# Kernel optimization log

Measured on AMD Instinct MI355X. Metric: run time of the kernel, lower is better.

The kernel has to match this reference:

```python
import jax, jax.numpy as jnp
from jax import lax
import numpy as np

P1, P2, M1, M2, WIN, STEP = 7, 7, 18, 55, 37, 4


def _unfold(x, p):
    # x: [N,C,Hp,Wp] -> [N, C*p*p, Ho*Wo], torch.nn.functional.unfold ordering (C, di, dj)
    N, C, Hp, Wp = x.shape
    Ho, Wo = Hp - p + 1, Wp - p + 1
    cols = jnp.stack([x[:, :, i:i + Ho, j:j + Wo] for i in range(p) for j in range(p)], axis=2)
    return cols.reshape(N, C * p * p, Ho * Wo)


def _reflect_unfold(x, r, p):
    return _unfold(jnp.pad(x, ((0, 0), (0, 0), (r, r), (r, r)), mode='reflect'), p)


def _fold(X, p, oh, ow):
    # inverse of unfold (sum of overlapping patches), torch.nn.functional.fold
    N, n, L = X.shape
    Ho, Wo = oh - p + 1, ow - p + 1
    C = n // (p * p)
    Xr = X.reshape(N, C, p, p, Ho, Wo)
    out = jnp.zeros((N, C, oh, ow), X.dtype)
    for i in range(p):
        for j in range(p):
            out = out.at[:, :, i:i + Ho, j:j + Wo].add(Xr[:, :, i, j])
    return out


def _block_matching(x, m, p, w, s):
    # x: [N,1,H,W] -> flat patch indices [N, B*m] into the (H+w-1)x(W+w-1) unfold grid
    N, C, H, Wd = x.shape
    inc = w // 2
    xs = _reflect_unfold(x, p // 2 + inc, p).reshape(N, p * p, H + 2 * inc, Wd + 2 * inc)
    xc = xs[:, :, inc:inc + H:s, inc:inc + Wd:s]  # [N, p*p, Hs, Ws]
    Hs, Ws = xc.shape[2], xc.shape[3]
    offs = jnp.stack(jnp.meshgrid(jnp.arange(w), jnp.arange(w), indexing='ij'), axis=-1).reshape(-1, 2)
    def d_of(off):
        xo = lax.dynamic_slice(xs, (0, 0, off[0], off[1]), (N, p * p, H, Wd))[:, :, ::s, ::s]
        return jnp.sum((xo - xc) ** 2, axis=1)  # [N, Hs, Ws]
    dist = jnp.moveaxis(lax.map(d_of, offs), 0, 1)  # [N, w*w, Hs, Ws]
    dist = dist.at[:, inc * w + inc].set(-1.0)  # force self-match first
    _, idx = lax.top_k(-jnp.transpose(dist, (0, 2, 3, 1)), m)  # smallest m, sorted
    idx = jnp.transpose(idx, (0, 3, 1, 2))  # [N, m, Hs, Ws]
    ir = idx // w - inc
    ic = idx % w - inc
    rows = inc + s * jnp.arange(Hs)
    cols = inc + s * jnp.arange(Ws)
    flat = (ir + rows[None, None, :, None]) * (Wd + w - 1) + (ic + cols[None, None, None, :])
    return jnp.transpose(flat.reshape(N, m, Hs * Ws), (0, 2, 1)).reshape(N, -1)  # [N, B*m]


def _group_patches(unf, idx, m, n):
    # unf: [N, n, L], idx: [N, B*m] -> [N, B, m, n]
    N = unf.shape[0]
    g = jnp.take_along_axis(unf, idx[:, None, :], axis=2)  # [N, n, B*m]
    return jnp.transpose(g, (0, 2, 1)).reshape(N, -1, m, n)


def _denoise1(Y, sigma):
    m, n = Y.shape[2], Y.shape[3]
    YtY = jnp.einsum('abik,abjk->abij', Y, Y)
    rhs = YtY - (n * sigma ** 2) * jnp.eye(m, dtype=Y.dtype)
    theta = jnp.swapaxes(jnp.linalg.solve(YtY, rhs), -1, -2)
    Xh = theta @ Y
    wts = 1.0 / jnp.sum(theta ** 2, axis=3, keepdims=True)
    return Xh, wts


def _denoise2(Y, X, sigma):
    m, n = X.shape[2], X.shape[3]
    XtX = jnp.einsum('abik,abjk->abij', X, X)
    A = XtX + (n * sigma ** 2) * jnp.eye(m, dtype=X.dtype)
    theta = jnp.swapaxes(jnp.linalg.solve(A, XtX), -1, -2)
    Xh = theta @ Y
    wts = 1.0 / jnp.sum(theta ** 2, axis=3, keepdims=True)
    return Xh, wts


def _aggregation(Y, wts, idx, H, Wd, L, p, w):
    # Y: [N,B,m,n], wts: [N,B,m,1], idx: [N,B*m]; scatter-add into unfold grid, fold, normalize
    N, B, m, n = Y.shape
    Yw = jnp.transpose(Y * wts, (0, 3, 1, 2)).reshape(N, n, B * m)
    wflat = jnp.broadcast_to(wts.reshape(N, 1, B * m), (N, n, B * m))
    def scat(vals, ib):
        return jnp.zeros((n, L), vals.dtype).at[:, ib].add(vals)
    Xsum = jax.vmap(scat)(Yw, idx)
    div = jax.vmap(scat)(wflat, idx)
    oh, ow = H + w - 1 + p - 1, Wd + w - 1 + p - 1
    num = _fold(Xsum, p, oh, ow)
    den = _fold(div, p, oh, ow)
    r = w // 2 + p // 2
    return (num / den)[:, :, r:-r, r:-r]


def _nlridge(input_y, sigma):
    N, C, H, Wd = input_y.shape
    w, s = WIN, STEP
    # ---- step 1 ----
    p, m = P1, M1
    yb = jnp.mean(input_y, axis=1, keepdims=True)
    idx1 = _block_matching(lax.stop_gradient(yb), m, p, w, s)
    unf_y1 = _reflect_unfold(input_y, p // 2 + w // 2, p)
    Y1 = _group_patches(unf_y1, idx1, m, C * p * p)
    Xh1, w1 = _denoise1(Y1, sigma)
    den1 = _aggregation(Xh1, w1, idx1, H, Wd, unf_y1.shape[2], p, w)
    # ---- step 2 ----
    p, m = P2, M2
    xb = jnp.mean(den1, axis=1, keepdims=True)
    idx2 = _block_matching(lax.stop_gradient(xb), m, p, w, s)
    unf_y2 = _reflect_unfold(input_y, p // 2 + w // 2, p)
    unf_x2 = _reflect_unfold(den1, p // 2 + w // 2, p)
    Y2 = _group_patches(unf_y2, idx2, m, C * p * p)
    X2 = _group_patches(unf_x2, idx2, m, C * p * p)
    Xh2, w2 = _denoise2(Y2, X2, sigma)
    return _aggregation(Xh2, w2, idx2, H, Wd, unf_y2.shape[2], p, w)


def setup_inputs() -> dict:
    key = jax.random.key(0)
    k1 = jax.random.fold_in(key, 1)
    input_y = jax.random.uniform(k1, (1, 1, 256, 256), dtype=jnp.float32)
    sigma = jnp.asarray(0.1, dtype=jnp.float32)  # ~25/255 AWGN
    return {"input_y": input_y, "sigma": sigma}


def reference(input_y, sigma):
    return _nlridge(input_y, sigma)
```

## Files before the change

kernel.cpp:

```cpp
#include <hip/hip_runtime.h>
#include <math.h>
#include <float.h>

constexpr int IMG  = 256;
constexpr int PADR = 21;
constexpr int PDIM = IMG + 2*PADR;
constexpr int XDIM = PDIM - 7 + 1;
constexpr int LTOT = XDIM * XDIM;
constexpr int WSZ  = 37;
constexpr int INC  = 18;
constexpr int ST   = 4;
constexpr int GDIM = 64;
constexpr int NBLK = GDIM * GDIM;
constexpr int PS   = 7;
constexpr int PP   = 49;
constexpr int MM1  = 18;
constexpr int MM2  = 55;
constexpr int RG   = 43;
constexpr int NOFF = WSZ * WSZ;
constexpr int UCAP = (NOFF + 63) / 64;
constexpr int TDIM = 43;
constexpr int TSZ  = TDIM * TDIM;
constexpr int SLABSTRIDE = 2 * TSZ;

__global__ void pad_reflect(const float* __restrict__ src, float* __restrict__ dst)
{
    int idx = blockIdx.x * 256 + threadIdx.x;
    if (idx >= PDIM * PDIM) return;
    int y = idx / PDIM, x = idx % PDIM;
    int oy = y - PADR; oy = (oy < 0) ? -oy : ((oy >= IMG) ? 2*(IMG-1) - oy : oy);
    int ox = x - PADR; ox = (ox < 0) ? -ox : ((ox >= IMG) ? 2*(IMG-1) - ox : ox);
    dst[idx] = src[oy * IMG + ox];
}

__global__ __launch_bounds__(256) void block_match(const float* __restrict__ pad,
                                                   int* __restrict__ pos, int m)
{
    __shared__ float reg[RG][RG + 1];
    __shared__ float dist[NOFF];

    const int gi = blockIdx.y, gj = blockIdx.x;
    const int tid = threadIdx.x;
    const int r0 = ST * gi, c0 = ST * gj;

    for (int t = tid; t < RG * RG; t += 256) {
        int r = t / RG, c = t % RG;
        reg[r][c] = pad[(r0 + r) * PDIM + (c0 + c)];
    }
    __syncthreads();

    float q[PP];
#pragma unroll
    for (int i = 0; i < PS; i++)
#pragma unroll
        for (int j = 0; j < PS; j++)
            q[i * PS + j] = reg[INC + i][INC + j];

    for (int o = tid; o < NOFF; o += 256) {
        int oi = o / WSZ, oj = o % WSZ;
        float s = 0.f;
#pragma unroll
        for (int i = 0; i < PS; i++)
#pragma unroll
            for (int j = 0; j < PS; j++) {
                float d = reg[oi + i][oj + j] - q[i * PS + j];
                s += d * d;
            }
        dist[o] = (o == INC * WSZ + INC) ? -1.0f : s;
    }
    __syncthreads();

    if (tid >= 64) return;
    const int lane = tid;

    float dv[UCAP];
#pragma unroll
    for (int u = 0; u < UCAP; u++) {
        int o = lane + (u << 6);
        dv[u] = (o < NOFF) ? dist[o] : FLT_MAX;
    }

    const int blk = gi * GDIM + gj;
    for (int sel = 0; sel < m; sel++) {
        float bv = dv[0]; int bo = lane;
#pragma unroll
        for (int u = 1; u < UCAP; u++) {
            int o = lane + (u << 6);
            if (dv[u] < bv) { bv = dv[u]; bo = o; }
        }
#pragma unroll
        for (int d = 1; d < 64; d <<= 1) {
            float ov = __shfl_xor(bv, d);
            int   oo = __shfl_xor(bo, d);
            if (ov < bv || (ov == bv && oo < bo)) { bv = ov; bo = oo; }
        }
        if (lane == 0) {
            int oi = bo / WSZ, oj = bo % WSZ;
            pos[blk * m + sel] = (oi + ST * gi) * XDIM + (oj + ST * gj);
        }
#pragma unroll
        for (int u = 0; u < UCAP; u++)
            if (bo == lane + (u << 6)) dv[u] = FLT_MAX;
    }
}

template<int M_, bool ADDC, bool SLAB>
__global__ __launch_bounds__(256) void denoise_scatter(
    const float* __restrict__ padY, const float* __restrict__ padS,
    const int* __restrict__ pos, const float* __restrict__ sigma_p,
    float* __restrict__ dst, float* __restrict__ Wacc)
{
    constexpr int MP = (M_ + 4) & ~3;
    constexpr int SS = 52;
    constexpr int YS = 60;

    __shared__ __align__(16) float Ssh[M_ * SS];
    __shared__ __align__(16) float Yt [PP * YS];
    __shared__ __align__(16) float Msh[M_ * MP];
    __shared__ float tile[SLAB ? 2 * TSZ : 1];
    __shared__ float wsh[M_];
    __shared__ int   posh[M_];

    const int tid = threadIdx.x;
    const int blk = blockIdx.x;
    const float sg = *sigma_p;
    const float c  = (float)PP * sg * sg;

    if (tid < M_) posh[tid] = pos[blk * M_ + tid];
    if (SLAB)
        for (int t = tid; t < 2 * TSZ; t += 256) tile[t] = 0.f;
    __syncthreads();

    for (int t = tid; t < M_ * SS; t += 256) {
        int k = t / SS, qq = t - k * SS;
        float v = 0.f;
        if (qq < PP) {
            int p_ = posh[k];
            int a = p_ / XDIM, b = p_ - (p_ / XDIM) * XDIM;
            v = padS[(a + qq / PS) * PDIM + (b + qq % PS)];
        }
        Ssh[t] = v;
    }
    for (int t = tid; t < PP * M_; t += 256) {
        int qq = t / M_, k = t - qq * M_;
        int p_ = posh[k];
        int a = p_ / XDIM, b = p_ - (p_ / XDIM) * XDIM;
        Yt[qq * YS + k] = padY[(a + qq / PS) * PDIM + (b + qq % PS)];
    }
    __syncthreads();

    for (int t = tid; t < M_ * M_; t += 256) {
        int i = t / M_, j = t - i * M_;
        if (j > i) continue;
        const float4* Si = (const float4*)&Ssh[i * SS];
        const float4* Sj = (const float4*)&Ssh[j * SS];
        float acc = 0.f;
#pragma unroll
        for (int cch = 0; cch < SS / 4; cch++) {
            float4 a4 = Si[cch], b4 = Sj[cch];
            acc += a4.x * b4.x + a4.y * b4.y + a4.z * b4.z + a4.w * b4.w;
        }
        if (ADDC && i == j) acc += c;
        Msh[i * MP + j] = acc;
    }
    __syncthreads();

    if (tid < 64) {
        const int j = (tid < M_) ? tid : (M_ - 1);
        float col[M_];
#pragma unroll
        for (int i = 0; i < M_; i++)
            col[i] = Msh[(i >= j) ? (i * MP + j) : (j * MP + i)];

#pragma unroll
        for (int k = 0; k < M_; k++) {
            float d = __int_as_float(__builtin_amdgcn_readlane(__float_as_int(col[k]), k));
            d = (fabsf(d) > 1e-30f) ? d : 1e-30f;
            float dinv = 1.0f / d;
            float cks = col[k];
            float f  = (j == k) ? (1.0f - dinv) : (cks * dinv);
            float fn = -f;
#pragma unroll
            for (int i = 0; i < M_; i++) {
                if (i == k) continue;
                float aik = __int_as_float(__builtin_amdgcn_readlane(__float_as_int(cks), i));
                col[i] = fmaf(aik, fn, col[i]);
            }
            col[k] = (j == k) ? (-dinv) : (cks * dinv);
        }
        if (tid < M_) {
            float s = 0.f;
#pragma unroll
            for (int i = 0; i < M_; i++) {
                float th = fmaf(c, col[i], (i == j) ? 1.f : 0.f);
                s = fmaf(th, th, s);
            }
            wsh[j] = 1.0f / s;
#pragma unroll
            for (int i = 0; i < M_; i++)
                Msh[i * MP + j] = -col[i];
        }
    }
    __syncthreads();

    const int r0 = ST * (blk >> 6), c0 = ST * (blk & (GDIM - 1));
    for (int t = tid; t < M_ * PP; t += 256) {
        int k = t / PP, qq = t - k * PP;
        const float4* Mi = (const float4*)&Msh[k * MP];
        const float4* Yq = (const float4*)&Yt [qq * YS];
        float z = 0.f;
#pragma unroll
        for (int cch = 0; cch < M_ / 4; cch++) {
            float4 a4 = Mi[cch], b4 = Yq[cch];
            z += a4.x * b4.x + a4.y * b4.y + a4.z * b4.z + a4.w * b4.w;
        }
#pragma unroll
        for (int jj = (M_ / 4) * 4; jj < M_; jj++)
            z += Msh[k * MP + jj] * Yt[qq * YS + jj];
        float xh = Yt[qq * YS + k] - c * z;
        float wk = wsh[k];
        int p_ = posh[k];
        if (SLAB) {
            int a = p_ / XDIM, b = p_ - (p_ / XDIM) * XDIM;
            int loc = (a - r0 + qq / PS) * TDIM + (b - c0 + qq % PS);
            atomicAdd(&tile[loc], xh * wk);
            atomicAdd(&tile[TSZ + loc], wk);
        } else {
            atomicAdd(&dst[qq * LTOT + p_], xh * wk);
        }
    }
    if (SLAB) {
        __syncthreads();
        float* g = dst + (size_t)blk * SLABSTRIDE;
        for (int t = tid; t < 2 * TSZ; t += 256) g[t] = tile[t];
    } else {
        for (int t = tid; t < M_; t += 256)
            atomicAdd(&Wacc[posh[t]], wsh[t]);
    }
}

__global__ void fold_slab(const float* __restrict__ slab, float* __restrict__ out)
{
    int idx = blockIdx.x * 256 + threadIdx.x;
    if (idx >= IMG * IMG) return;
    int y = (idx >> 8) + PADR, x = (idx & 255) + PADR;
    int qy = y >> 2, ry = y & 3;
    int qx = x >> 2, rx = x & 3;
    float num = 0.f, den = 0.f;
    for (int di = 0; di < 11; di++) {
        int gi = qy - di;
        int li = 4 * di + ry;
        if ((unsigned)gi > (unsigned)(GDIM - 1) || li >= TDIM) continue;
        for (int dj = 0; dj < 11; dj++) {
            int gj = qx - dj;
            int lj = 4 * dj + rx;
            if ((unsigned)gj > (unsigned)(GDIM - 1) || lj >= TDIM) continue;
            const float* s = slab + (size_t)((gi << 6) + gj) * SLABSTRIDE + li * TDIM + lj;
            num += s[0];
            den += s[TSZ];
        }
    }
    out[idx] = num / den;
}

__global__ void fold_norm(const float* __restrict__ Xsum, const float* __restrict__ Wacc,
                          float* __restrict__ out)
{
    int idx = blockIdx.x * 256 + threadIdx.x;
    if (idx >= IMG * IMG) return;
    int y0 = idx / IMG, x0 = idx % IMG;
    int y = y0 + PADR, x = x0 + PADR;
    float num = 0.f, den = 0.f;
#pragma unroll
    for (int i = 0; i < PS; i++)
#pragma unroll
        for (int j = 0; j < PS; j++) {
            int a = y - i, b = x - j;
            num += Xsum[(i * PS + j) * LTOT + a * XDIM + b];
            den += Wacc[a * XDIM + b];
        }
    out[idx] = num / den;
}

extern "C" void kernel_launch(void* const* d_in, const int* in_sizes, int n_in,
                              void* d_out, int out_size, void* d_ws, size_t ws_size,
                              hipStream_t stream)
{
    const float* input = (const float*)d_in[0];
    const float* sigma = (const float*)d_in[1];
    float* out = (float*)d_out;

    char* ws = (char*)d_ws;
    float* padY = (float*)ws; ws += (size_t)PDIM * PDIM * 4;
    float* padX = (float*)ws; ws += (size_t)PDIM * PDIM * 4;
    float* den1 = (float*)ws; ws += (size_t)IMG * IMG * 4;
    int*   pos  = (int*)ws;   ws += (size_t)NBLK * MM2 * 4;
    size_t head = (size_t)(ws - (char*)d_ws);
    size_t slabBytes = (size_t)NBLK * SLABSTRIDE * 4;

    const int padBlocks = (PDIM * PDIM + 255) / 256;
    const int imgBlocks = (IMG * IMG + 255) / 256;

    if (ws_size >= head + slabBytes) {
        float* slab = (float*)ws;

        pad_reflect<<<padBlocks, 256, 0, stream>>>(input, padY);
        block_match<<<dim3(GDIM, GDIM), 256, 0, stream>>>(padY, pos, MM1);
        denoise_scatter<MM1, false, true><<<NBLK, 256, 0, stream>>>(padY, padY, pos, sigma,
                                                                    slab, nullptr);
        fold_slab<<<imgBlocks, 256, 0, stream>>>(slab, den1);

        pad_reflect<<<padBlocks, 256, 0, stream>>>(den1, padX);
        block_match<<<dim3(GDIM, GDIM), 256, 0, stream>>>(padX, pos, MM2);
        denoise_scatter<MM2, true, true><<<NBLK, 256, 0, stream>>>(padY, padX, pos, sigma,
                                                                   slab, nullptr);
        fold_slab<<<imgBlocks, 256, 0, stream>>>(slab, out);
    } else {
        float* Xsum = (float*)ws; ws += (size_t)PP * LTOT * 4;
        float* Wacc = (float*)ws;

        hipMemsetAsync(Xsum, 0, (size_t)PP * LTOT * 4, stream);
        hipMemsetAsync(Wacc, 0, (size_t)LTOT * 4, stream);
        pad_reflect<<<padBlocks, 256, 0, stream>>>(input, padY);
        block_match<<<dim3(GDIM, GDIM), 256, 0, stream>>>(padY, pos, MM1);
        denoise_scatter<MM1, false, false><<<NBLK, 256, 0, stream>>>(padY, padY, pos, sigma,
                                                                     Xsum, Wacc);
        fold_norm<<<imgBlocks, 256, 0, stream>>>(Xsum, Wacc, den1);

        pad_reflect<<<padBlocks, 256, 0, stream>>>(den1, padX);
        hipMemsetAsync(Xsum, 0, (size_t)PP * LTOT * 4, stream);
        hipMemsetAsync(Wacc, 0, (size_t)LTOT * 4, stream);
        block_match<<<dim3(GDIM, GDIM), 256, 0, stream>>>(padX, pos, MM2);
        denoise_scatter<MM2, true, false><<<NBLK, 256, 0, stream>>>(padY, padX, pos, sigma,
                                                                    Xsum, Wacc);
        fold_norm<<<imgBlocks, 256, 0, stream>>>(Xsum, Wacc, out);
    }
}
```

Baseline: 1.305 ms.

## Overlap Gauss-Jordan inversion with Y loads and register-tile the reconstruction

Wave 0 now runs the Gauss-Jordan inversion as a rolled loop, broadcasting each pivot column through shared memory. Meanwhile the other three waves load the Y patches and zero the accumulation tile, so that load work overlaps the serial inversion. The S buffer and the slab tile now share one shared-memory region to cut LDS footprint. The final M*Y product is tiled 2x2 per thread to reuse shared-memory operands. This adds a shared-memory round trip per pivot step and some padding and bounds logic.

```diff
diff --git a/kernel.cpp b/kernel.cpp
--- a/kernel.cpp
+++ b/kernel.cpp
@@ -113,13 +113,17 @@
     constexpr int MP = (M_ + 4) & ~3;
     constexpr int SS = 52;
     constexpr int YS = 60;
-
-    __shared__ __align__(16) float Ssh[M_ * SS];
+    constexpr int UN = (2 * TSZ > M_ * SS) ? 2 * TSZ : M_ * SS;
+
     __shared__ __align__(16) float Yt [PP * YS];
     __shared__ __align__(16) float Msh[M_ * MP];
-    __shared__ float tile[SLAB ? 2 * TSZ : 1];
+    __shared__ __align__(16) float SorT[UN];
+    __shared__ float pcol[M_];
     __shared__ float wsh[M_];
     __shared__ int   posh[M_];
+
+    float* Ssh  = SorT;
+    float* tile = SorT;
 
     const int tid = threadIdx.x;
     const int blk = blockIdx.x;
@@ -127,12 +131,10 @@
     const float c  = (float)PP * sg * sg;
 
     if (tid < M_) posh[tid] = pos[blk * M_ + tid];
-    if (SLAB)
-        for (int t = tid; t < 2 * TSZ; t += 256) tile[t] = 0.f;
     __syncthreads();
 
     for (int t = tid; t < M_ * SS; t += 256) {
-        int k = t / SS, qq = t - k * SS;
+        int k = t / SS, qq = t - (t / SS) * SS;
         float v = 0.f;
         if (qq < PP) {
             int p_ = posh[k];
@@ -141,16 +143,10 @@
         }
         Ssh[t] = v;
     }
-    for (int t = tid; t < PP * M_; t += 256) {
-        int qq = t / M_, k = t - qq * M_;
-        int p_ = posh[k];
-        int a = p_ / XDIM, b = p_ - (p_ / XDIM) * XDIM;
-        Yt[qq * YS + k] = padY[(a + qq / PS) * PDIM + (b + qq % PS)];
-    }
     __syncthreads();
 
     for (int t = tid; t < M_ * M_; t += 256) {
-        int i = t / M_, j = t - i * M_;
+        int i = t / M_, j = t - (t / M_) * M_;
         if (j > i) continue;
         const float4* Si = (const float4*)&Ssh[i * SS];
         const float4* Sj = (const float4*)&Ssh[j * SS];
@@ -172,21 +168,27 @@
         for (int i = 0; i < M_; i++)
             col[i] = Msh[(i >= j) ? (i * MP + j) : (j * MP + i)];
 
-#pragma unroll
+#pragma unroll 1
         for (int k = 0; k < M_; k++) {
-            float d = __int_as_float(__builtin_amdgcn_readlane(__float_as_int(col[k]), k));
+            if (tid == k) {
+#pragma unroll
+                for (int i = 0; i < M_; i++) pcol[i] = col[i];
+            }
+            float piv = pcol[j];
+            float d   = pcol[k];
             d = (fabsf(d) > 1e-30f) ? d : 1e-30f;
             float dinv = 1.0f / d;
-            float cks = col[k];
-            float f  = (j == k) ? (1.0f - dinv) : (cks * dinv);
-            float fn = -f;
+            bool  isk  = (j == k);
+            float f    = isk ? (1.0f - dinv) : (piv * dinv);
+            float fix  = isk ? (-dinv)       : (piv * dinv);
+            float negf = -f;
 #pragma unroll
             for (int i = 0; i < M_; i++) {
-                if (i == k) continue;
-                float aik = __int_as_float(__builtin_amdgcn_readlane(__float_as_int(cks), i));
-                col[i] = fmaf(aik, fn, col[i]);
-            }
-            col[k] = (j == k) ? (-dinv) : (cks * dinv);
+                float b   = __int_as_float(
+                    __builtin_amdgcn_readlane(__float_as_int(col[i]), k));
+                float upd = fmaf(b, negf, col[i]);
+                col[i] = (i == k) ? fix : upd;
+            }
         }
         if (tid < M_) {
             float s = 0.f;
@@ -199,34 +201,80 @@
 #pragma unroll
             for (int i = 0; i < M_; i++)
                 Msh[i * MP + j] = -col[i];
-        }
-    }
-    __syncthreads();
-
+        } else if (tid < MP) {
+#pragma unroll
+            for (int i = 0; i < M_; i++)
+                Msh[i * MP + tid] = 0.f;
+        }
+    } else {
+        const int t0 = tid - 64;
+        for (int t = t0; t < PP * MP; t += 192) {
+            int qq = t / MP, k = t - (t / MP) * MP;
+            float v = 0.f;
+            if (k < M_) {
+                int p_ = posh[k];
+                int a = p_ / XDIM, b = p_ - (p_ / XDIM) * XDIM;
+                v = padY[(a + qq / PS) * PDIM + (b + qq % PS)];
+            }
+            Yt[qq * YS + k] = v;
+        }
+        if (SLAB)
+            for (int t = t0; t < 2 * TSZ; t += 192) tile[t] = 0.f;
+    }
+    __syncthreads();
+
+    constexpr int KP = (M_ + 1) / 2;
+    constexpr int QP = (PP + 1) / 2;
     const int r0 = ST * (blk >> 6), c0 = ST * (blk & (GDIM - 1));
-    for (int t = tid; t < M_ * PP; t += 256) {
-        int k = t / PP, qq = t - k * PP;
-        const float4* Mi = (const float4*)&Msh[k * MP];
-        const float4* Yq = (const float4*)&Yt [qq * YS];
-        float z = 0.f;
-#pragma unroll
-        for (int cch = 0; cch < M_ / 4; cch++) {
-            float4 a4 = Mi[cch], b4 = Yq[cch];
-            z += a4.x * b4.x + a4.y * b4.y + a4.z * b4.z + a4.w * b4.w;
-        }
-#pragma unroll
-        for (int jj = (M_ / 4) * 4; jj < M_; jj++)
-            z += Msh[k * MP + jj] * Yt[qq * YS + jj];
-        float xh = Yt[qq * YS + k] - c * z;
-        float wk = wsh[k];
-        int p_ = posh[k];
+    for (int t = tid; t < KP * QP; t += 256) {
+        int kp = t / QP, qp = t - (t / QP) * QP;
+        int k0 = kp * 2, k1 = k0 + 1;
+        int qq0 = qp * 2, qq1 = qq0 + 1;
+        bool k1v = (k1 < M_), q1v = (qq1 < PP);
+        int k1c  = k1v ? k1 : k0;
+        int qq1c = q1v ? qq1 : qq0;
+        const float4* G0 = (const float4*)&Msh[k0  * MP];
+        const float4* G1 = (const float4*)&Msh[k1c * MP];
+        const float4* Y0 = (const float4*)&Yt [qq0  * YS];
+        const float4* Y1 = (const float4*)&Yt [qq1c * YS];
+        float z00 = 0.f, z01 = 0.f, z10 = 0.f, z11 = 0.f;
+#pragma unroll
+        for (int cch = 0; cch < MP / 4; cch++) {
+            float4 g0 = G0[cch], g1 = G1[cch], y0 = Y0[cch], y1 = Y1[cch];
+            z00 += g0.x*y0.x + g0.y*y0.y + g0.z*y0.z + g0.w*y0.w;
+            z01 += g0.x*y1.x + g0.y*y1.y + g0.z*y1.z + g0.w*y1.w;
+            z10 += g1.x*y0.x + g1.y*y0.y + g1.z*y0.z + g1.w*y0.w;
+            z11 += g1.x*y1.x + g1.y*y1.y + g1.z*y1.z + g1.w*y1.w;
+        }
+        float w0 = wsh[k0], w1 = k1v ? wsh[k1] : 0.f;
+        int p0 = posh[k0], p1 = posh[k1c];
+        float xh00 = (Yt[qq0  * YS + k0 ] - c * z00) * w0;
+        float xh01 = (Yt[qq1c * YS + k0 ] - c * z01) * w0;
+        float xh10 = (Yt[qq0  * YS + k1c] - c * z10) * w1;
+        float xh11 = (Yt[qq1c * YS + k1c] - c * z11) * w1;
+        int a0 = p0 / XDIM, b0 = p0 - (p0 / XDIM) * XDIM;
+        int a1 = p1 / XDIM, b1 = p1 - (p1 / XDIM) * XDIM;
+        int i0 = qq0 / PS, j0 = qq0 - i0 * PS;
+        int i1 = qq1 / PS, j1 = qq1 - i1 * PS;
         if (SLAB) {
-            int a = p_ / XDIM, b = p_ - (p_ / XDIM) * XDIM;
-            int loc = (a - r0 + qq / PS) * TDIM + (b - c0 + qq % PS);
-            atomicAdd(&tile[loc], xh * wk);
-            atomicAdd(&tile[TSZ + loc], wk);
+            int u0 = a0 - r0, v0 = b0 - c0, u1 = a1 - r0, v1 = b1 - c0;
+            int l00 = (u0 + i0) * TDIM + v0 + j0;
+            int l10 = (u1 + i0) * TDIM + v1 + j0;
+            atomicAdd(&tile[l00], xh00); atomicAdd(&tile[TSZ + l00], w0);
+            atomicAdd(&tile[l10], xh10); atomicAdd(&tile[TSZ + l10], w1);
+            if (q1v) {
+                int l01 = (u0 + i1) * TDIM + v0 + j1;
+                int l11 = (u1 + i1) * TDIM + v1 + j1;
+                atomicAdd(&tile[l01], xh01); atomicAdd(&tile[TSZ + l01], w0);
+                atomicAdd(&tile[l11], xh11); atomicAdd(&tile[TSZ + l11], w1);
+            }
         } else {
-            atomicAdd(&dst[qq * LTOT + p_], xh * wk);
+            atomicAdd(&dst[qq0 * LTOT + p0], xh00);
+            if (q1v) atomicAdd(&dst[qq1 * LTOT + p0], xh01);
+            if (k1v) {
+                atomicAdd(&dst[qq0 * LTOT + p1], xh10);
+                if (q1v) atomicAdd(&dst[qq1 * LTOT + p1], xh11);
+            }
         }
     }
     if (SLAB) {
```

Result: faster. 1.096 ms (-16.0%).
